# Performance work log

Measured on AMD Instinct MI355X. Metric: run time of the kernel, lower is better.

The kernel has to match this reference:

```python
import jax, jax.numpy as jnp
import numpy as np

B, S, D, H = 4, 2048, 1024, 16
HD = D // H  # head_dim = 64


def setup_inputs() -> dict:
    key = jax.random.key(0)
    ks = jax.random.split(key, 4)
    scale = 0.02
    return {
        "x": jax.random.normal(ks[0], (B, S, D), dtype=jnp.float32),
        "W_attn": jax.random.normal(ks[1], (D, 3 * D), dtype=jnp.float32) * scale,
        "b_attn": jnp.zeros((3 * D,), dtype=jnp.float32),
        "W_proj": jax.random.normal(ks[2], (D, D), dtype=jnp.float32) * scale,
        "b_proj": jnp.zeros((D,), dtype=jnp.float32),
    }


def reference(x, W_attn, b_attn, W_proj, b_proj):
    b, s, d = x.shape
    qkv = x @ W_attn + b_attn                      # [b, s, 3d]
    q, k, v = jnp.split(qkv, 3, axis=2)
    # [b, s, d] -> [b, h, s, hd]
    def to_heads(t):
        return t.reshape(b, s, H, HD).transpose(0, 2, 1, 3)
    q, k, v = to_heads(q), to_heads(k), to_heads(v)
    scores = jnp.einsum("bhqd,bhkd->bhqk", q, k) / jnp.sqrt(jnp.float32(HD))
    causal = jnp.tril(jnp.ones((s, s), dtype=bool))  # [s, s]
    scores = jnp.where(causal[None, None], scores, jnp.float32(-jnp.inf))
    probs = jax.nn.softmax(scores, axis=-1)
    y = jnp.einsum("bhqk,bhkd->bhqd", probs, v)    # [b, h, s, hd]
    y = y.transpose(0, 2, 1, 3).reshape(b, s, d)
    return y @ W_proj + b_proj
```

## Files before the change

kernel.cpp:

```cpp
#include <hip/hip_runtime.h>
#include <hip/hip_bf16.h>
#include <type_traits>

#define SQ    2048
#define DIM   1024
#define NH    16
#define HDIM  64
#define BATCH 4

typedef unsigned short u16;
typedef __bf16 bf16x8 __attribute__((ext_vector_type(8)));
typedef float  f32x4  __attribute__((ext_vector_type(4)));
typedef u16    u16x8  __attribute__((ext_vector_type(8)));

#define QSCALE 0.180336880f

__device__ __forceinline__ u16 f2bf(float f) {
  union { float f; unsigned u; } v; v.f = f;
  unsigned r = v.u + 0x7fffu + ((v.u >> 16) & 1u);
  return (u16)(r >> 16);
}

__device__ __forceinline__ float fast_exp2(float x) {
#if __has_builtin(__builtin_amdgcn_exp2f)
  return __builtin_amdgcn_exp2f(x);
#else
  float y;
  asm("v_exp_f32 %0, %1" : "=v"(y) : "v"(x));
  return y;
#endif
}

__device__ __forceinline__ void gll16(const u16* g, u16* l) {
  __builtin_amdgcn_global_load_lds((const __attribute__((address_space(1))) void*)g,
                                   (__attribute__((address_space(3))) void*)l,
                                   16, 0, 0);
}

__global__ __launch_bounds__(256)
void f32_to_bf16_vec(const float* __restrict__ in, u16* __restrict__ out, int n4)
{
  const int i = blockIdx.x * blockDim.x + threadIdx.x;
  if (i < n4) {
    const float4 v = ((const float4*)in)[i];
    ushort4 o;
    o.x = f2bf(v.x); o.y = f2bf(v.y); o.z = f2bf(v.z); o.w = f2bf(v.w);
    ((ushort4*)out)[i] = o;
  }
}

__global__ void transpose_f32_bf16(const float* __restrict__ in, u16* __restrict__ out,
                                   int R, int C)
{
  __shared__ u16 tile[32][33];
  const int bx = blockIdx.x * 32, by = blockIdx.y * 32;
  const int tx = threadIdx.x, ty = threadIdx.y;
  #pragma unroll
  for (int i = 0; i < 32; i += 8)
    tile[ty + i][tx] = f2bf(in[(size_t)(by + ty + i) * C + bx + tx]);
  __syncthreads();
  #pragma unroll
  for (int i = 0; i < 32; i += 8)
    out[(size_t)(bx + ty + i) * R + by + tx] = tile[tx][ty + i];
}

template<int MODE>
__global__ __launch_bounds__(256)
void gemm_bt(const u16* __restrict__ A, const u16* __restrict__ Bt,
             const float* __restrict__ bias, int K,
             u16* __restrict__ o0, u16* __restrict__ o1, float* __restrict__ of)
{
  __shared__ __align__(16) u16 A0[128 * 32], A1[128 * 32];
  __shared__ __align__(16) u16 B0[128 * 32], B1[128 * 32];

  const int t    = threadIdx.x;
  const int lane = t & 63, wave = t >> 6;
  const int l15  = lane & 15, quad = lane >> 4;
  const int wm   = (wave & 1) * 64, wn = (wave >> 1) * 64;
  const int m0   = blockIdx.y * 128, n0 = blockIdx.x * 128;

  const int srow = wave * 32 + (lane >> 2);
  const int scol = (lane & 3) * 8;

  f32x4 acc[4][4] = {};

  for (int k0 = 0; k0 < K; k0 += 64) {
    const u16* ga = A  + (size_t)(m0 + srow) * K + k0 + scol;
    const u16* gb = Bt + (size_t)(n0 + srow) * K + k0 + scol;
    gll16(ga,              &A0[(wave * 32)      * 32]);
    gll16(ga + 32,         &A1[(wave * 32)      * 32]);
    gll16(ga + 16 * K,     &A0[(wave * 32 + 16) * 32]);
    gll16(ga + 16 * K + 32,&A1[(wave * 32 + 16) * 32]);
    gll16(gb,              &B0[(wave * 32)      * 32]);
    gll16(gb + 32,         &B1[(wave * 32)      * 32]);
    gll16(gb + 16 * K,     &B0[(wave * 32 + 16) * 32]);
    gll16(gb + 16 * K + 32,&B1[(wave * 32 + 16) * 32]);
    __syncthreads();

    #pragma unroll
    for (int ks = 0; ks < 2; ++ks) {
      const u16* Als = ks ? A1 : A0;
      const u16* Bls = ks ? B1 : B0;
      bf16x8 af[4], bfr[4];
      #pragma unroll
      for (int i = 0; i < 4; ++i) af[i]  = *(const bf16x8*)&Als[(wm + 16*i + l15) * 32 + quad * 8];
      #pragma unroll
      for (int j = 0; j < 4; ++j) bfr[j] = *(const bf16x8*)&Bls[(wn + 16*j + l15) * 32 + quad * 8];
      #pragma unroll
      for (int i = 0; i < 4; ++i)
        #pragma unroll
        for (int j = 0; j < 4; ++j)
          acc[i][j] = (MODE == 2)
            ? __builtin_amdgcn_mfma_f32_16x16x32_bf16(bfr[j], af[i], acc[i][j], 0, 0, 0)
            : __builtin_amdgcn_mfma_f32_16x16x32_bf16(af[i], bfr[j], acc[i][j], 0, 0, 0);
    }
    __syncthreads();
  }

  if (MODE == 2) {
    #pragma unroll
    for (int j = 0; j < 4; ++j) {
      #pragma unroll
      for (int r = 0; r < 4; ++r) {
        const int d = n0 + wn + 16*j + quad * 4 + r;
        const float bn = bias[d];
        const int h = d >> 6, hd = d & 63;
        #pragma unroll
        for (int i = 0; i < 4; ++i) {
          const int m = m0 + wm + 16*i + l15;
          const int b = m >> 11, s = m & 2047;
          o0[(((size_t)(b * NH + h)) * HDIM + hd) * SQ + s] = f2bf(acc[i][j][r] + bn);
        }
      }
    }
  } else {
    #pragma unroll
    for (int j = 0; j < 4; ++j) {
      const int n = n0 + wn + 16*j + l15;
      const float bn = bias[n];
      #pragma unroll
      for (int i = 0; i < 4; ++i) {
        #pragma unroll
        for (int r = 0; r < 4; ++r) {
          const int m = m0 + wm + 16*i + quad * 4 + r;
          const float val = acc[i][j][r] + bn;
          if (MODE == 1) {
            const int sec = n >> 10, d = n & 1023;
            const int h = d >> 6, hd = d & 63;
            const int b = m >> 11, s = m & 2047;
            const int bh = b * NH + h;
            if (sec == 0) o0[((size_t)bh * SQ + s) * HDIM + hd] = f2bf(val * QSCALE);
            else          o1[((size_t)bh * SQ + s) * HDIM + hd] = f2bf(val);
          } else {
            of[(size_t)m * DIM + n] = val;
          }
        }
      }
    }
  }
}

#define LP 72

__global__ __launch_bounds__(256)
void attn_fused(const u16* __restrict__ q_ws, const u16* __restrict__ k_ws,
                const u16* __restrict__ v_t, u16* __restrict__ y_ws)
{
  __shared__ __align__(16) u16 Kls[2][2][64 * 32];
  __shared__ __align__(16) u16 Vls[2][2][64 * 32];
  __shared__ __align__(16) u16 Pls[4][32 * LP];

  const int bh = blockIdx.x;
  const int p  = blockIdx.y;
  const int b = bh >> 4, h = bh & 15;
  const int t = threadIdx.x;
  const int lane = t & 63, wave = t >> 6;
  const int l15 = lane & 15, quad = lane >> 4;

  const u16* Q  = q_ws + (size_t)bh * SQ * HDIM;
  const u16* Kp = k_ws + (size_t)bh * SQ * HDIM;
  const u16* Vp = v_t  + (size_t)bh * HDIM * SQ;

  const int qtH = 15 - p, qtL = p;
  const int qrowH = qtH * 128 + wave * 32;
  const int qrowL = qtL * 128 + wave * 32;

  bf16x8 qf[4][2];
  #pragma unroll
  for (int qi = 0; qi < 2; ++qi)
    #pragma unroll
    for (int ks = 0; ks < 2; ++ks) {
      qf[qi][ks]     = *(const bf16x8*)&Q[(size_t)(qrowH + 16*qi + l15) * HDIM + ks * 32 + quad * 8];
      qf[2 + qi][ks] = *(const bf16x8*)&Q[(size_t)(qrowL + 16*qi + l15) * HDIM + ks * 32 + quad * 8];
    }

  f32x4 o[4][4] = {};
  float l_q[4] = {};

  const int sr = wave * 16 + (lane >> 2);
  const int sc = (lane & 3) * 8;

  auto stage = [&](int kv0, int buf) {
    gll16(&Kp[(size_t)(kv0 + sr) * HDIM + sc],      &Kls[buf][0][wave * 512]);
    gll16(&Kp[(size_t)(kv0 + sr) * HDIM + sc + 32], &Kls[buf][1][wave * 512]);
    gll16(&Vp[(size_t)sr * SQ + kv0 + sc],          &Vls[buf][0][wave * 512]);
    gll16(&Vp[(size_t)sr * SQ + kv0 + sc + 32],     &Vls[buf][1][wave * 512]);
  };

  auto compute = [&](int kv0, int buf, int base, int qrow, auto maskc) {
    constexpr bool MASKED = decltype(maskc)::value;
    f32x4 st[4][2] = {};
    #pragma unroll
    for (int ks = 0; ks < 2; ++ks) {
      const u16* Kh = Kls[buf][ks];
      #pragma unroll
      for (int kt = 0; kt < 4; ++kt) {
        bf16x8 kf = *(const bf16x8*)&Kh[(16*kt + l15) * 32 + quad * 8];
        #pragma unroll
        for (int qi = 0; qi < 2; ++qi)
          st[kt][qi] = __builtin_amdgcn_mfma_f32_16x16x32_bf16(kf, qf[base + qi][ks], st[kt][qi], 0, 0, 0);
      }
    }

    #pragma unroll
    for (int qi = 0; qi < 2; ++qi) {
      const int q = qrow + 16*qi + l15;
      float rsum = 0.f;
      #pragma unroll
      for (int kt = 0; kt < 4; ++kt)
        #pragma unroll
        for (int r = 0; r < 4; ++r) {
          float pv = fast_exp2(st[kt][qi][r]);
          if (MASKED && (kv0 + 16*kt + quad*4 + r) > q) pv = 0.f;
          st[kt][qi][r] = pv;
          rsum += pv;
        }
      l_q[base + qi] += rsum;
    }

    #pragma unroll
    for (int qi = 0; qi < 2; ++qi)
      #pragma unroll
      for (int kt = 0; kt < 4; ++kt) {
        union { __hip_bfloat162 h2[2]; ushort4 u4; } pk;
        pk.h2[0] = __float22bfloat162_rn(make_float2(st[kt][qi][0], st[kt][qi][1]));
        pk.h2[1] = __float22bfloat162_rn(make_float2(st[kt][qi][2], st[kt][qi][3]));
        *(ushort4*)&Pls[wave][(16*qi + l15) * LP + 16*kt + quad * 4] = pk.u4;
      }

    #pragma unroll
    for (int ks = 0; ks < 2; ++ks) {
      const u16* Vh = Vls[buf][ks];
      bf16x8 vf[4];
      #pragma unroll
      for (int n = 0; n < 4; ++n)
        vf[n] = *(const bf16x8*)&Vh[(16*n + l15) * 32 + quad * 8];
      #pragma unroll
      for (int mi = 0; mi < 2; ++mi) {
        bf16x8 pa = *(const bf16x8*)&Pls[wave][(16*mi + l15) * LP + ks * 32 + quad * 8];
        #pragma unroll
        for (int n = 0; n < 4; ++n)
          o[base + mi][n] = __builtin_amdgcn_mfma_f32_16x16x32_bf16(pa, vf[n], o[base + mi][n], 0, 0, 0);
      }
    }
  };

  const int ntiles = 2 * qtH + 2;
  const int lastH  = 2 * qtH + (wave >> 1);
  const int lastL  = 2 * qtL + (wave >> 1);

  stage(0, 0);
  for (int kvt = 0; kvt < ntiles; ++kvt) {
    const int cur = kvt & 1;
    const int kv0 = kvt * 64;
    __syncthreads();
    if (kvt + 1 < ntiles) stage((kvt + 1) * 64, cur ^ 1);
    if (kvt < lastH)       compute(kv0, cur, 0, qrowH, std::integral_constant<bool,false>{});
    else if (kvt == lastH) compute(kv0, cur, 0, qrowH, std::integral_constant<bool,true>{});
    if (kvt < lastL)       compute(kv0, cur, 2, qrowL, std::integral_constant<bool,false>{});
    else if (kvt == lastL) compute(kv0, cur, 2, qrowL, std::integral_constant<bool,true>{});
  }

  #pragma unroll
  for (int s = 0; s < 4; ++s) {
    l_q[s] += __shfl_xor(l_q[s], 16);
    l_q[s] += __shfl_xor(l_q[s], 32);
  }
  #pragma unroll
  for (int g = 0; g < 2; ++g) {
    const int qrow = g ? qrowL : qrowH;
    const int base = g * 2;
    #pragma unroll
    for (int mi = 0; mi < 2; ++mi)
      #pragma unroll
      for (int r = 0; r < 4; ++r) {
        const float lr = __shfl(l_q[base + mi], quad * 4 + r);
        const float inv = 1.0f / lr;
        const int qg = qrow + 16*mi + quad * 4 + r;
        #pragma unroll
        for (int n = 0; n < 4; ++n)
          y_ws[((size_t)b * SQ + qg) * DIM + h * HDIM + 16*n + l15] = f2bf(o[base + mi][n][r] * inv);
      }
  }
}

extern "C" void kernel_launch(void* const* d_in, const int* in_sizes, int n_in,
                              void* d_out, int out_size, void* d_ws, size_t ws_size,
                              hipStream_t stream)
{
  const float* x      = (const float*)d_in[0];
  const float* W_attn = (const float*)d_in[1];
  const float* b_attn = (const float*)d_in[2];
  const float* W_proj = (const float*)d_in[3];
  const float* b_proj = (const float*)d_in[4];
  float* out = (float*)d_out;

  char* ws = (char*)d_ws;
  u16* WattnT = (u16*)(ws);
  u16* WprojT = (u16*)(ws + 6291456);
  u16* xb     = (u16*)(ws + 8388608);
  u16* y_ws   = xb;
  u16* q_ws   = (u16*)(ws + 25165824);
  u16* k_ws   = (u16*)(ws + 41943040);
  u16* v_tw   = (u16*)(ws + 58720256);

  const dim3 tb(32, 8);
  transpose_f32_bf16<<<dim3(3 * DIM / 32, DIM / 32), tb, 0, stream>>>(W_attn, WattnT, DIM, 3 * DIM);
  transpose_f32_bf16<<<dim3(DIM / 32, DIM / 32), tb, 0, stream>>>(W_proj, WprojT, DIM, DIM);
  f32_to_bf16_vec<<<(BATCH * SQ * DIM / 4 + 255) / 256, 256, 0, stream>>>(x, xb, BATCH * SQ * DIM / 4);

  gemm_bt<1><<<dim3(2 * DIM / 128, BATCH * SQ / 128), 256, 0, stream>>>(
      xb, WattnT, b_attn, DIM, q_ws, k_ws, nullptr);
  gemm_bt<2><<<dim3(DIM / 128, BATCH * SQ / 128), 256, 0, stream>>>(
      xb, WattnT + (size_t)2048 * DIM, b_attn + 2048, DIM, v_tw, nullptr, nullptr);

  attn_fused<<<dim3(BATCH * NH, 8), 256, 0, stream>>>(q_ws, k_ws, v_tw, y_ws);

  gemm_bt<0><<<dim3(DIM / 128, BATCH * SQ / 128), 256, 0, stream>>>(
      y_ws, WprojT, b_proj, DIM, nullptr, nullptr, out);
}
```

Measured before the change: 267.8 us.

## XOR-swizzle K/V/P shared tiles into 64-wide rows and raise MFMA priority

Replaces the split 32-column K/V LDS halves and the padded P buffer with unpadded 64-column tiles that use an XOR swizzle on the 8-element column chunk. Global-to-LDS staging, the K/V fragment reads and the P writes and reads all use the matching swizzled offsets. The aim is to avoid LDS bank conflicts without padding and to shrink LDS use. It also wraps the MFMA sections in s_setprio so waves doing matrix work get scheduling priority, which may change how well the waves interleave.

```diff
diff --git a/kernel.cpp b/kernel.cpp
--- a/kernel.cpp
+++ b/kernel.cpp
@@ -160,15 +160,13 @@
   }
 }
 
-#define LP 72
-
 __global__ __launch_bounds__(256)
 void attn_fused(const u16* __restrict__ q_ws, const u16* __restrict__ k_ws,
                 const u16* __restrict__ v_t, u16* __restrict__ y_ws)
 {
-  __shared__ __align__(16) u16 Kls[2][2][64 * 32];
-  __shared__ __align__(16) u16 Vls[2][2][64 * 32];
-  __shared__ __align__(16) u16 Pls[4][32 * LP];
+  __shared__ __align__(16) u16 Kls[2][64 * 64];
+  __shared__ __align__(16) u16 Vls[2][64 * 64];
+  __shared__ __align__(16) u16 Pls[4][32 * 64];
 
   const int bh = blockIdx.x;
   const int p  = blockIdx.y;
@@ -176,6 +174,10 @@
   const int t = threadIdx.x;
   const int lane = t & 63, wave = t >> 6;
   const int l15 = lane & 15, quad = lane >> 4;
+  const int rx  = l15 & 7;
+  const int cK0 = ((quad      ^ rx) << 3);
+  const int cK1 = (((quad | 4) ^ rx) << 3);
+  const int pswz = rx << 3;
 
   const u16* Q  = q_ws + (size_t)bh * SQ * HDIM;
   const u16* Kp = k_ws + (size_t)bh * SQ * HDIM;
@@ -197,30 +199,34 @@
   f32x4 o[4][4] = {};
   float l_q[4] = {};
 
-  const int sr = wave * 16 + (lane >> 2);
-  const int sc = (lane & 3) * 8;
+  const int r3   = lane >> 3;
+  const int c8   = lane & 7;
+  const int scol = ((c8 ^ r3) << 3);
 
   auto stage = [&](int kv0, int buf) {
-    gll16(&Kp[(size_t)(kv0 + sr) * HDIM + sc],      &Kls[buf][0][wave * 512]);
-    gll16(&Kp[(size_t)(kv0 + sr) * HDIM + sc + 32], &Kls[buf][1][wave * 512]);
-    gll16(&Vp[(size_t)sr * SQ + kv0 + sc],          &Vls[buf][0][wave * 512]);
-    gll16(&Vp[(size_t)sr * SQ + kv0 + sc + 32],     &Vls[buf][1][wave * 512]);
+    gll16(&Kp[(size_t)(kv0 + wave*16     + r3) * HDIM + scol], &Kls[buf][(wave*16    ) * 64]);
+    gll16(&Kp[(size_t)(kv0 + wave*16 + 8 + r3) * HDIM + scol], &Kls[buf][(wave*16 + 8) * 64]);
+    gll16(&Vp[(size_t)(wave*16     + r3) * SQ + kv0 + scol],   &Vls[buf][(wave*16    ) * 64]);
+    gll16(&Vp[(size_t)(wave*16 + 8 + r3) * SQ + kv0 + scol],   &Vls[buf][(wave*16 + 8) * 64]);
   };
 
   auto compute = [&](int kv0, int buf, int base, int qrow, auto maskc) {
     constexpr bool MASKED = decltype(maskc)::value;
     f32x4 st[4][2] = {};
+    const u16* Kb = Kls[buf];
+    __builtin_amdgcn_s_setprio(1);
     #pragma unroll
     for (int ks = 0; ks < 2; ++ks) {
-      const u16* Kh = Kls[buf][ks];
+      const int cs = ks ? cK1 : cK0;
       #pragma unroll
       for (int kt = 0; kt < 4; ++kt) {
-        bf16x8 kf = *(const bf16x8*)&Kh[(16*kt + l15) * 32 + quad * 8];
+        bf16x8 kf = *(const bf16x8*)&Kb[(16*kt + l15) * 64 + cs];
         #pragma unroll
         for (int qi = 0; qi < 2; ++qi)
           st[kt][qi] = __builtin_amdgcn_mfma_f32_16x16x32_bf16(kf, qf[base + qi][ks], st[kt][qi], 0, 0, 0);
       }
     }
+    __builtin_amdgcn_s_setprio(0);
 
     #pragma unroll
     for (int qi = 0; qi < 2; ++qi) {
@@ -245,24 +251,27 @@
         union { __hip_bfloat162 h2[2]; ushort4 u4; } pk;
         pk.h2[0] = __float22bfloat162_rn(make_float2(st[kt][qi][0], st[kt][qi][1]));
         pk.h2[1] = __float22bfloat162_rn(make_float2(st[kt][qi][2], st[kt][qi][3]));
-        *(ushort4*)&Pls[wave][(16*qi + l15) * LP + 16*kt + quad * 4] = pk.u4;
-      }
-
+        *(ushort4*)&Pls[wave][(16*qi + l15) * 64 + ((16*kt + quad*4) ^ pswz)] = pk.u4;
+      }
+
+    const u16* Vb = Vls[buf];
+    __builtin_amdgcn_s_setprio(1);
     #pragma unroll
     for (int ks = 0; ks < 2; ++ks) {
-      const u16* Vh = Vls[buf][ks];
+      const int cs = ks ? cK1 : cK0;
       bf16x8 vf[4];
       #pragma unroll
       for (int n = 0; n < 4; ++n)
-        vf[n] = *(const bf16x8*)&Vh[(16*n + l15) * 32 + quad * 8];
+        vf[n] = *(const bf16x8*)&Vb[(16*n + l15) * 64 + cs];
       #pragma unroll
       for (int mi = 0; mi < 2; ++mi) {
-        bf16x8 pa = *(const bf16x8*)&Pls[wave][(16*mi + l15) * LP + ks * 32 + quad * 8];
+        bf16x8 pa = *(const bf16x8*)&Pls[wave][(16*mi + l15) * 64 + ((ks*32 + quad*8) ^ pswz)];
         #pragma unroll
         for (int n = 0; n < 4; ++n)
           o[base + mi][n] = __builtin_amdgcn_mfma_f32_16x16x32_bf16(pa, vf[n], o[base + mi][n], 0, 0, 0);
       }
     }
+    __builtin_amdgcn_s_setprio(0);
   };
 
   const int ntiles = 2 * qtH + 2;
```

Result: faster. 259.2 us (-3.2%).
